# Kernel tuning notes

Hardware: AMD Instinct MI355X
Metric: run time of the kernel (lower is better)

Reference implementation:

```python
import jax, jax.numpy as jnp
import numpy as np

DIM = 256
HEADS = 8
WINDOWS = (1, 2, 4)
B, H, W = 1, 64, 64


def _integral(a):
    # double cumsum over last two dims, then zero-pad one row/col at top/left
    s = jnp.cumsum(jnp.cumsum(a, axis=-2), axis=-1)
    pad = [(0, 0)] * (a.ndim - 2) + [(1, 0), (1, 0)]
    return jnp.pad(s, pad)


def _box(P, ws, Ho, Wo):
    # replicate-pad then box-difference; equivalent to the 2x2 [[1,-1],[-1,1]]
    # kernel conv2d with dilation=ws applied in the torch module.
    tp = ws - 1
    r = tp // 2
    l = tp - r
    pad = [(0, 0)] * (P.ndim - 2) + [(l, r), (l, r)]
    Pp = jnp.pad(P, pad, mode='edge')
    return (Pp[..., ws:ws + Ho, ws:ws + Wo] - Pp[..., ws:ws + Ho, :Wo]
            - Pp[..., :Ho, ws:ws + Wo] + Pp[..., :Ho, :Wo])


def setup_inputs() -> dict:
    key = jax.random.key(0)
    ks = jax.random.split(key, 6)
    x = jax.random.normal(ks[0], (B, DIM, H, W), jnp.float32)
    Wq = jax.random.normal(ks[1], (DIM, DIM), jnp.float32) * 0.05
    Wk = jax.random.normal(ks[2], (DIM, DIM), jnp.float32) * 0.05
    Wv = jax.random.normal(ks[3], (DIM, DIM), jnp.float32) * 0.05
    Wout = jax.random.normal(ks[4], (DIM, DIM * len(WINDOWS)), jnp.float32) * 0.05
    bout = jnp.zeros((DIM,), jnp.float32)
    return {"x": x, "Wq": Wq, "Wk": Wk, "Wv": Wv, "Wout": Wout, "bout": bout}


def reference(x, Wq, Wk, Wv, Wout, bout):
    b, C, Hh, Ww = x.shape
    h = HEADS
    d = C // h
    # 1x1 convs (no bias)
    q = jnp.einsum('bchw,oc->bohw', x, Wq).reshape(b * h, d, Hh, Ww)
    k = jnp.einsum('bchw,oc->bohw', x, Wk).reshape(b * h, d, Hh, Ww)
    v = jnp.einsum('bchw,oc->bohw', x, Wv).reshape(b * h, d, Hh, Ww)
    q = jax.nn.sigmoid(q)
    k = jax.nn.sigmoid(k)
    v = v / jnp.maximum(jnp.linalg.norm(v, axis=1, keepdims=True), 1e-12)

    Ik = _integral(k)                                  # (bh, d, H+1, W+1)
    Ikv = _integral(jnp.einsum('bfhw,bghw->bfghw', k, v))  # (bh, d, d, H+1, W+1)

    outs = []
    for w in WINDOWS:
        ws = Hh // w
        wk = _box(Ik, ws, Hh, Ww)    # (bh, d, H, W)
        wkv = _box(Ikv, ws, Hh, Ww)  # (bh, d, d, H, W)
        attn = jnp.einsum('bdhw,bdfhw->bfhw', q, wkv)
        norm = jnp.einsum('bdhw,bdhw->bhw', q, wk)
        attn = attn / (norm[:, None] + 1e-6)
        outs.append(attn.reshape(b, C, Hh, Ww))
    o = jnp.concatenate(outs, axis=1)  # (b, C*len(WINDOWS), H, W)
    return jnp.einsum('bchw,oc->bohw', o, Wout) + bout[None, :, None, None]
```

## Files before the change

### kernel.cpp

```cpp
#include <hip/hip_runtime.h>
#include <math.h>

#define NPIX 4096
#define CHSZ 3145728
#define NRMSZ 98304

template <int CTRL, int RM>
__device__ __forceinline__ float dpp_add(float x) {
    int xi = __builtin_bit_cast(int, x);
    int sh = __builtin_amdgcn_update_dpp(0, xi, CTRL, RM, 0xf, false);
    return x + __builtin_bit_cast(float, sh);
}

__device__ __forceinline__ float wave_iscan(float x) {
    x = dpp_add<0x111, 0xf>(x);
    x = dpp_add<0x112, 0xf>(x);
    x = dpp_add<0x114, 0xf>(x);
    x = dpp_add<0x118, 0xf>(x);
    x = dpp_add<0x142, 0xa>(x);
    x = dpp_add<0x143, 0xc>(x);
    return x;
}

__device__ __forceinline__ void lds_barrier() {
    asm volatile("s_waitcnt lgkmcnt(0)" ::: "memory");
    __builtin_amdgcn_s_barrier();
    __builtin_amdgcn_sched_barrier(0);
}

__global__ __launch_bounds__(256) void qkv_kernel(
    const float* __restrict__ x, const float* __restrict__ Wq,
    const float* __restrict__ Wk, const float* __restrict__ Wv,
    float* __restrict__ qo, float* __restrict__ ko, float* __restrict__ vo)
{
    const int pt = blockIdx.x * 128;
    const int ot = blockIdx.y * 32;
    const int mat = blockIdx.z;
    const float* __restrict__ W = (mat == 0) ? Wq : ((mat == 1) ? Wk : Wv);
    float* __restrict__ out = (mat == 0) ? qo : ((mat == 1) ? ko : vo);

    __shared__ __align__(16) float Xs[32][132];
    __shared__ __align__(16) float Wt[32][36];

    const int t = threadIdx.x;
    const int pc = t & 31;
    const int oc = t >> 5;
    const int xc = t >> 5;
    const int xp = (t & 31) << 2;
    const int lo = t >> 3;
    const int lg = (t & 7) << 2;

    float4 xf[4];
    float4 wf;
#pragma unroll
    for (int i = 0; i < 4; i++)
        xf[i] = *reinterpret_cast<const float4*>(x + (xc + 8 * i) * NPIX + pt + xp);
    wf = *reinterpret_cast<const float4*>(W + (ot + lo) * 256 + lg);

    float acc[4][4];
#pragma unroll
    for (int j = 0; j < 4; j++)
#pragma unroll
        for (int i = 0; i < 4; i++) acc[j][i] = 0.f;

    for (int kt = 0; kt < 256; kt += 32) {
#pragma unroll
        for (int i = 0; i < 4; i++)
            *reinterpret_cast<float4*>(&Xs[xc + 8 * i][xp]) = xf[i];
        Wt[lg + 0][lo] = wf.x;
        Wt[lg + 1][lo] = wf.y;
        Wt[lg + 2][lo] = wf.z;
        Wt[lg + 3][lo] = wf.w;
        __syncthreads();
        if (kt + 32 < 256) {
#pragma unroll
            for (int i = 0; i < 4; i++)
                xf[i] = *reinterpret_cast<const float4*>(
                    x + (kt + 32 + xc + 8 * i) * NPIX + pt + xp);
            wf = *reinterpret_cast<const float4*>(W + (ot + lo) * 256 + kt + 32 + lg);
        }
#pragma unroll
        for (int kk = 0; kk < 32; kk++) {
            float4 a = *reinterpret_cast<const float4*>(&Xs[kk][pc << 2]);
            float av[4] = {a.x, a.y, a.z, a.w};
            float4 b4 = *reinterpret_cast<const float4*>(&Wt[kk][oc << 2]);
            float bv[4] = {b4.x, b4.y, b4.z, b4.w};
#pragma unroll
            for (int j = 0; j < 4; j++)
#pragma unroll
                for (int i = 0; i < 4; i++)
                    acc[j][i] = fmaf(bv[j], av[i], acc[j][i]);
        }
        __syncthreads();
    }

    if (mat < 2) {
#pragma unroll
        for (int j = 0; j < 4; j++) {
            const int o = ot + (oc << 2) + j;
            float4 r;
            r.x = 1.f / (1.f + __expf(-acc[j][0]));
            r.y = 1.f / (1.f + __expf(-acc[j][1]));
            r.z = 1.f / (1.f + __expf(-acc[j][2]));
            r.w = 1.f / (1.f + __expf(-acc[j][3]));
            *reinterpret_cast<float4*>(out + o * NPIX + pt + (pc << 2)) = r;
        }
    } else {
        float* scratch = &Xs[0][0];
        __syncthreads();
#pragma unroll
        for (int i = 0; i < 4; i++) {
            float ss = 0.f;
#pragma unroll
            for (int j = 0; j < 4; j++) ss += acc[j][i] * acc[j][i];
            scratch[oc * 128 + (pc << 2) + i] = ss;
        }
        __syncthreads();
        float scale[4];
#pragma unroll
        for (int i = 0; i < 4; i++) {
            float tot = 0.f;
#pragma unroll
            for (int g = 0; g < 8; g++) tot += scratch[g * 128 + (pc << 2) + i];
            scale[i] = 1.f / fmaxf(sqrtf(tot), 1e-12f);
        }
#pragma unroll
        for (int j = 0; j < 4; j++) {
            const int o = ot + (oc << 2) + j;
            float4 r;
            r.x = acc[j][0] * scale[0];
            r.y = acc[j][1] * scale[1];
            r.z = acc[j][2] * scale[2];
            r.w = acc[j][3] * scale[3];
            *reinterpret_cast<float4*>(out + o * NPIX + pt + (pc << 2)) = r;
        }
    }
}

template <int PD>
__global__ __launch_bounds__(512) void attn_kernel(
    const float* __restrict__ q, const float* __restrict__ k,
    const float* __restrict__ v, float* __restrict__ num, float* __restrict__ nrm)
{
    const int f = blockIdx.x;
    const int head = blockIdx.y;
    const int dg = blockIdx.z;
    const bool isnorm = (f == 32);

    const float* __restrict__ kh = k + (head * 32 + dg * PD) * NPIX;
    const float* __restrict__ qh = q + (head * 32 + dg * PD) * NPIX;
    const float* __restrict__ vf = v + (head * 32 + (isnorm ? 0 : f)) * NPIX;

    __shared__ __align__(16) float Pt[65][132];
    __shared__ float csum[8][68];

    const int t = threadIdx.x;
    const int lane = t & 63;
    const int wv = t >> 6;

    for (int i = t; i < 65 * 132; i += 512) (&Pt[0][0])[i] = 0.f;

    float vreg[8], kcur[8];
#pragma unroll
    for (int i = 0; i < 8; i++) {
        const int r = wv * 8 + i;
        vreg[i] = isnorm ? 1.f : vf[r * 64 + lane];
        kcur[i] = kh[r * 64 + lane];
    }

    float acc[3][8];
#pragma unroll
    for (int w = 0; w < 3; w++)
#pragma unroll
        for (int i = 0; i < 8; i++) acc[w][i] = 0.f;

    lds_barrier();

    for (int dd = 0; dd < PD; dd++) {
        float qv[8];
#pragma unroll
        for (int g = 0; g < 2; g++)
#pragma unroll
            for (int j = 0; j < 4; j++)
                qv[g * 4 + j] = qh[dd * NPIX + ((wv + 8 * g) * 4 + j) * 64 + lane];

        float pv[8];
        float run = 0.f;
#pragma unroll
        for (int i = 0; i < 8; i++) {
            float rs = wave_iscan(kcur[i] * vreg[i]);
            pv[i] = run;
            run += rs;
        }
        if (dd + 1 < PD) {
#pragma unroll
            for (int i = 0; i < 8; i++)
                kcur[i] = kh[(dd + 1) * NPIX + (wv * 8 + i) * 64 + lane];
        }
        csum[wv][lane] = run;
        lds_barrier();
        float off = 0.f;
#pragma unroll
        for (int w2 = 0; w2 < 7; w2++) if (w2 < wv) off += csum[w2][lane];
#pragma unroll
        for (int i = 0; i < 8; i++) pv[i] += off;
#pragma unroll
        for (int s = 0; s < 2; s++) {
            float4 r4 = make_float4(pv[4 * s], pv[4 * s + 1], pv[4 * s + 2], pv[4 * s + 3]);
            *reinterpret_cast<float4*>(&Pt[lane + 1][32 + wv * 8 + 4 * s]) = r4;
        }
        if (wv == 7) {
            const float tot = off + run;
            const float4 p4 = make_float4(tot, tot, tot, tot);
#pragma unroll
            for (int s = 0; s < 8; s++)
                *reinterpret_cast<float4*>(&Pt[lane + 1][96 + 4 * s]) = p4;
        }
        lds_barrier();
#pragma unroll
        for (int g = 0; g < 2; g++) {
            const int y0 = (wv + 8 * g) * 4;
#pragma unroll
            for (int w = 0; w < 3; w++) {
                const int hw = 32 >> w;
                const int xlo = max(lane - hw, 0);
                const int xhi = min(lane + hw, 64);
                const int ylo = 32 + y0 - hw;
                const int yhi = 32 + y0 + hw;
                float4 A4 = *reinterpret_cast<const float4*>(&Pt[xhi][yhi]);
                float4 B4 = *reinterpret_cast<const float4*>(&Pt[xlo][yhi]);
                float4 C4, E4;
                if (y0 + 3 <= hw) {
                    C4 = make_float4(0.f, 0.f, 0.f, 0.f);
                    E4 = C4;
                } else {
                    C4 = *reinterpret_cast<const float4*>(&Pt[xhi][ylo]);
                    E4 = *reinterpret_cast<const float4*>(&Pt[xlo][ylo]);
                }
                acc[w][g * 4 + 0] = fmaf(qv[g * 4 + 0], (A4.x - B4.x) - (C4.x - E4.x), acc[w][g * 4 + 0]);
                acc[w][g * 4 + 1] = fmaf(qv[g * 4 + 1], (A4.y - B4.y) - (C4.y - E4.y), acc[w][g * 4 + 1]);
                acc[w][g * 4 + 2] = fmaf(qv[g * 4 + 2], (A4.z - B4.z) - (C4.z - E4.z), acc[w][g * 4 + 2]);
                acc[w][g * 4 + 3] = fmaf(qv[g * 4 + 3], (A4.w - B4.w) - (C4.w - E4.w), acc[w][g * 4 + 3]);
            }
        }
    }

    float* __restrict__ nout = num + (size_t)dg * CHSZ;
    float* __restrict__ rout = nrm + (size_t)dg * NRMSZ;
#pragma unroll
    for (int w = 0; w < 3; w++) {
#pragma unroll
        for (int g = 0; g < 2; g++) {
#pragma unroll
            for (int j = 0; j < 4; j++) {
                const int px = ((wv + 8 * g) * 4 + j) * 64 + lane;
                const float val = acc[w][g * 4 + j];
                if (isnorm) rout[(w * 8 + head) * NPIX + px] = val;
                else        nout[((w * 8 + head) * 32 + f) * NPIX + px] = val;
            }
        }
    }
}

template <int NS>
__global__ __launch_bounds__(256) void out_kernel(
    const float* __restrict__ num, const float* __restrict__ nrm,
    const float* __restrict__ Wout, float* __restrict__ obuf)
{
    const int pt = blockIdx.x * 64;
    const int ot = blockIdx.y * 64;
    const int kt0 = blockIdx.z * 12;
    __shared__ __align__(16) float As[32][68];
    __shared__ __align__(16) float Wt[32][68];
    const int t = threadIdx.x;
    const int pc = t & 15;
    const int oc = t >> 4;
    const int xc = t >> 4;
    const int xp = (t & 15) << 2;
    const int lo = t & 63;
    const int lc = (t >> 6) << 2;

    float4 nv[NS][2], mv[NS], wf[2];
#pragma unroll
    for (int s = 0; s < NS; s++) {
#pragma unroll
        for (int i = 0; i < 2; i++)
            nv[s][i] = *reinterpret_cast<const float4*>(
                num + (size_t)s * CHSZ + (size_t)(kt0 * 32 + xc + 16 * i) * NPIX + pt + xp);
        mv[s] = *reinterpret_cast<const float4*>(
            nrm + (size_t)s * NRMSZ + kt0 * NPIX + pt + xp);
    }
    wf[0] = *reinterpret_cast<const float4*>(Wout + (ot + lo) * 768 + kt0 * 32 + lc);
    wf[1] = *reinterpret_cast<const float4*>(Wout + (ot + lo) * 768 + kt0 * 32 + lc + 16);

    float acc[4][4];
#pragma unroll
    for (int j = 0; j < 4; j++)
#pragma unroll
        for (int i = 0; i < 4; i++) acc[j][i] = 0.f;

    for (int kt = kt0; kt < kt0 + 12; kt++) {
        float4 ms = mv[0];
#pragma unroll
        for (int s = 1; s < NS; s++) {
            ms.x += mv[s].x; ms.y += mv[s].y; ms.z += mv[s].z; ms.w += mv[s].w;
        }
        float4 rv;
        rv.x = 1.f / (ms.x + 1e-6f); rv.y = 1.f / (ms.y + 1e-6f);
        rv.z = 1.f / (ms.z + 1e-6f); rv.w = 1.f / (ms.w + 1e-6f);
#pragma unroll
        for (int i = 0; i < 2; i++) {
            float4 r = nv[0][i];
#pragma unroll
            for (int s = 1; s < NS; s++) {
                r.x += nv[s][i].x; r.y += nv[s][i].y;
                r.z += nv[s][i].z; r.w += nv[s][i].w;
            }
            r.x *= rv.x; r.y *= rv.y; r.z *= rv.z; r.w *= rv.w;
            *reinterpret_cast<float4*>(&As[xc + 16 * i][xp]) = r;
        }
#pragma unroll
        for (int i = 0; i < 2; i++) {
            Wt[lc + 16 * i + 0][lo] = wf[i].x;
            Wt[lc + 16 * i + 1][lo] = wf[i].y;
            Wt[lc + 16 * i + 2][lo] = wf[i].z;
            Wt[lc + 16 * i + 3][lo] = wf[i].w;
        }
        __syncthreads();
        if (kt + 1 < kt0 + 12) {
#pragma unroll
            for (int s = 0; s < NS; s++) {
#pragma unroll
                for (int i = 0; i < 2; i++)
                    nv[s][i] = *reinterpret_cast<const float4*>(
                        num + (size_t)s * CHSZ +
                        (size_t)((kt + 1) * 32 + xc + 16 * i) * NPIX + pt + xp);
                mv[s] = *reinterpret_cast<const float4*>(
                    nrm + (size_t)s * NRMSZ + (kt + 1) * NPIX + pt + xp);
            }
            wf[0] = *reinterpret_cast<const float4*>(
                Wout + (ot + lo) * 768 + (kt + 1) * 32 + lc);
            wf[1] = *reinterpret_cast<const float4*>(
                Wout + (ot + lo) * 768 + (kt + 1) * 32 + lc + 16);
        }
#pragma unroll
        for (int kk = 0; kk < 32; kk++) {
            float4 a = *reinterpret_cast<const float4*>(&As[kk][pc << 2]);
            float av[4] = {a.x, a.y, a.z, a.w};
            float4 b4 = *reinterpret_cast<const float4*>(&Wt[kk][oc << 2]);
            float bv[4] = {b4.x, b4.y, b4.z, b4.w};
#pragma unroll
            for (int j = 0; j < 4; j++)
#pragma unroll
                for (int i = 0; i < 4; i++)
                    acc[j][i] = fmaf(bv[j], av[i], acc[j][i]);
        }
        __syncthreads();
    }

    float* __restrict__ ob = obuf + (size_t)blockIdx.z * 1048576;
#pragma unroll
    for (int j = 0; j < 4; j++) {
        const int o = ot + (oc << 2) + j;
        float4 r;
        r.x = acc[j][0]; r.y = acc[j][1]; r.z = acc[j][2]; r.w = acc[j][3];
        *reinterpret_cast<float4*>(ob + o * NPIX + pt + (pc << 2)) = r;
    }
}

__global__ __launch_bounds__(256) void kmerge_kernel(
    const float* __restrict__ obuf, const float* __restrict__ bout,
    float* __restrict__ out)
{
    const int i4 = (blockIdx.x * 256 + threadIdx.x) * 4;
    const float bb = bout[i4 >> 12];
    float4 a = *reinterpret_cast<const float4*>(obuf + i4);
    float4 b = *reinterpret_cast<const float4*>(obuf + 1048576 + i4);
    float4 r;
    r.x = a.x + b.x + bb;
    r.y = a.y + b.y + bb;
    r.z = a.z + b.z + bb;
    r.w = a.w + b.w + bb;
    *reinterpret_cast<float4*>(out + i4) = r;
}

extern "C" void kernel_launch(void* const* d_in, const int* in_sizes, int n_in,
                              void* d_out, int out_size, void* d_ws, size_t ws_size,
                              hipStream_t stream)
{
    const float* x    = (const float*)d_in[0];
    const float* Wq   = (const float*)d_in[1];
    const float* Wk   = (const float*)d_in[2];
    const float* Wv   = (const float*)d_in[3];
    const float* Wout = (const float*)d_in[4];
    const float* bout = (const float*)d_in[5];
    float* out = (float*)d_out;

    float* ws = (float*)d_ws;
    float* q   = ws;
    float* k   = ws + 1048576;
    float* v   = ws + 2097152;
    float* num = ws + 3145728;
    float* obuf = ws;
    const size_t fl = ws_size / 4;

    qkv_kernel<<<dim3(32, 8, 3), 256, 0, stream>>>(x, Wq, Wk, Wv, q, k, v);

    if (fl >= 3145728 + (size_t)4 * (CHSZ + NRMSZ)) {
        float* nrm = num + (size_t)4 * CHSZ;
        attn_kernel<8><<<dim3(33, 8, 4), 512, 0, stream>>>(q, k, v, num, nrm);
        out_kernel<4><<<dim3(64, 4, 2), 256, 0, stream>>>(num, nrm, Wout, obuf);
    } else if (fl >= 3145728 + (size_t)2 * (CHSZ + NRMSZ)) {
        float* nrm = num + (size_t)2 * CHSZ;
        attn_kernel<16><<<dim3(33, 8, 2), 512, 0, stream>>>(q, k, v, num, nrm);
        out_kernel<2><<<dim3(64, 4, 2), 256, 0, stream>>>(num, nrm, Wout, obuf);
    } else {
        float* nrm = num + CHSZ;
        attn_kernel<32><<<dim3(33, 8, 1), 512, 0, stream>>>(q, k, v, num, nrm);
        out_kernel<1><<<dim3(64, 4, 2), 256, 0, stream>>>(num, nrm, Wout, obuf);
    }
    kmerge_kernel<<<dim3(1024), 256, 0, stream>>>(obuf, bout, out);
}
```

Measured before the change: 141.7 us.

## Double-buffer prefix tile and software-pipeline scan to drop one barrier per step

The LDS prefix-sum tile and the column-sum scratch are double-buffered. The scan for step dd+1 is computed while step dd's box sums are read, which removes one workgroup barrier per iteration. The padded 132-wide tile, which replicated the total into 32 columns, is shrunk to 68 columns with a single total column, and the edge cases are handled by explicit branches. The trade is more registers (pvn, runn) and divergent branch paths in the inner loop.

```diff
diff --git a/kernel.cpp b/kernel.cpp
--- a/kernel.cpp
+++ b/kernel.cpp
@@ -151,14 +151,14 @@
     const float* __restrict__ qh = q + (head * 32 + dg * PD) * NPIX;
     const float* __restrict__ vf = v + (head * 32 + (isnorm ? 0 : f)) * NPIX;
 
-    __shared__ __align__(16) float Pt[65][132];
-    __shared__ float csum[8][68];
+    __shared__ __align__(16) float Pt[2][65][68];
+    __shared__ float csum[2][8][68];
 
     const int t = threadIdx.x;
     const int lane = t & 63;
     const int wv = t >> 6;
 
-    for (int i = t; i < 65 * 132; i += 512) (&Pt[0][0])[i] = 0.f;
+    for (int i = t; i < 2 * 65 * 68; i += 512) (&Pt[0][0][0])[i] = 0.f;
 
     float vreg[8], kcur[8];
 #pragma unroll
@@ -174,17 +174,8 @@
 #pragma unroll
         for (int i = 0; i < 8; i++) acc[w][i] = 0.f;
 
-    lds_barrier();
-
-    for (int dd = 0; dd < PD; dd++) {
-        float qv[8];
-#pragma unroll
-        for (int g = 0; g < 2; g++)
-#pragma unroll
-            for (int j = 0; j < 4; j++)
-                qv[g * 4 + j] = qh[dd * NPIX + ((wv + 8 * g) * 4 + j) * 64 + lane];
-
-        float pv[8];
+    float pv[8], runcur;
+    {
         float run = 0.f;
 #pragma unroll
         for (int i = 0; i < 8; i++) {
@@ -192,29 +183,50 @@
             pv[i] = run;
             run += rs;
         }
+        csum[0][wv][lane] = run;
+        runcur = run;
+        if (PD > 1) {
+#pragma unroll
+            for (int i = 0; i < 8; i++)
+                kcur[i] = kh[1 * NPIX + (wv * 8 + i) * 64 + lane];
+        }
+    }
+    lds_barrier();
+
+    float pvn[8], runn;
+    for (int dd = 0; dd < PD; dd++) {
+        const int b = dd & 1;
+        float off = 0.f;
+#pragma unroll
+        for (int w2 = 0; w2 < 7; w2++) if (w2 < wv) off += csum[b][w2][lane];
+#pragma unroll
+        for (int s = 0; s < 2; s++) {
+            float4 r4 = make_float4(pv[4 * s] + off, pv[4 * s + 1] + off,
+                                    pv[4 * s + 2] + off, pv[4 * s + 3] + off);
+            *reinterpret_cast<float4*>(&Pt[b][lane + 1][wv * 8 + 4 * s]) = r4;
+        }
+        if (wv == 7) Pt[b][lane + 1][64] = off + runcur;
+        float qv[8];
+#pragma unroll
+        for (int g = 0; g < 2; g++)
+#pragma unroll
+            for (int j = 0; j < 4; j++)
+                qv[g * 4 + j] = qh[dd * NPIX + ((wv + 8 * g) * 4 + j) * 64 + lane];
         if (dd + 1 < PD) {
-#pragma unroll
-            for (int i = 0; i < 8; i++)
-                kcur[i] = kh[(dd + 1) * NPIX + (wv * 8 + i) * 64 + lane];
-        }
-        csum[wv][lane] = run;
-        lds_barrier();
-        float off = 0.f;
-#pragma unroll
-        for (int w2 = 0; w2 < 7; w2++) if (w2 < wv) off += csum[w2][lane];
-#pragma unroll
-        for (int i = 0; i < 8; i++) pv[i] += off;
-#pragma unroll
-        for (int s = 0; s < 2; s++) {
-            float4 r4 = make_float4(pv[4 * s], pv[4 * s + 1], pv[4 * s + 2], pv[4 * s + 3]);
-            *reinterpret_cast<float4*>(&Pt[lane + 1][32 + wv * 8 + 4 * s]) = r4;
-        }
-        if (wv == 7) {
-            const float tot = off + run;
-            const float4 p4 = make_float4(tot, tot, tot, tot);
-#pragma unroll
-            for (int s = 0; s < 8; s++)
-                *reinterpret_cast<float4*>(&Pt[lane + 1][96 + 4 * s]) = p4;
+            float run = 0.f;
+#pragma unroll
+            for (int i = 0; i < 8; i++) {
+                float rs = wave_iscan(kcur[i] * vreg[i]);
+                pvn[i] = run;
+                run += rs;
+            }
+            csum[b ^ 1][wv][lane] = run;
+            runn = run;
+            if (dd + 2 < PD) {
+#pragma unroll
+                for (int i = 0; i < 8; i++)
+                    kcur[i] = kh[(dd + 2) * NPIX + (wv * 8 + i) * 64 + lane];
+            }
         }
         lds_barrier();
 #pragma unroll
@@ -225,23 +237,40 @@
                 const int hw = 32 >> w;
                 const int xlo = max(lane - hw, 0);
                 const int xhi = min(lane + hw, 64);
-                const int ylo = 32 + y0 - hw;
-                const int yhi = 32 + y0 + hw;
-                float4 A4 = *reinterpret_cast<const float4*>(&Pt[xhi][yhi]);
-                float4 B4 = *reinterpret_cast<const float4*>(&Pt[xlo][yhi]);
-                float4 C4, E4;
+                float c0, c1, c2, c3;
                 if (y0 + 3 <= hw) {
-                    C4 = make_float4(0.f, 0.f, 0.f, 0.f);
-                    E4 = C4;
+                    float4 A4 = *reinterpret_cast<const float4*>(&Pt[b][xhi][y0 + hw]);
+                    float4 B4 = *reinterpret_cast<const float4*>(&Pt[b][xlo][y0 + hw]);
+                    c0 = A4.x - B4.x; c1 = A4.y - B4.y;
+                    c2 = A4.z - B4.z; c3 = A4.w - B4.w;
+                } else if (y0 + hw >= 64) {
+                    float As = Pt[b][xhi][64];
+                    float Bs = Pt[b][xlo][64];
+                    float4 C4 = *reinterpret_cast<const float4*>(&Pt[b][xhi][y0 - hw]);
+                    float4 E4 = *reinterpret_cast<const float4*>(&Pt[b][xlo][y0 - hw]);
+                    const float ab = As - Bs;
+                    c0 = ab - (C4.x - E4.x); c1 = ab - (C4.y - E4.y);
+                    c2 = ab - (C4.z - E4.z); c3 = ab - (C4.w - E4.w);
                 } else {
-                    C4 = *reinterpret_cast<const float4*>(&Pt[xhi][ylo]);
-                    E4 = *reinterpret_cast<const float4*>(&Pt[xlo][ylo]);
+                    float4 A4 = *reinterpret_cast<const float4*>(&Pt[b][xhi][y0 + hw]);
+                    float4 B4 = *reinterpret_cast<const float4*>(&Pt[b][xlo][y0 + hw]);
+                    float4 C4 = *reinterpret_cast<const float4*>(&Pt[b][xhi][y0 - hw]);
+                    float4 E4 = *reinterpret_cast<const float4*>(&Pt[b][xlo][y0 - hw]);
+                    c0 = (A4.x - B4.x) - (C4.x - E4.x);
+                    c1 = (A4.y - B4.y) - (C4.y - E4.y);
+                    c2 = (A4.z - B4.z) - (C4.z - E4.z);
+                    c3 = (A4.w - B4.w) - (C4.w - E4.w);
                 }
-                acc[w][g * 4 + 0] = fmaf(qv[g * 4 + 0], (A4.x - B4.x) - (C4.x - E4.x), acc[w][g * 4 + 0]);
-                acc[w][g * 4 + 1] = fmaf(qv[g * 4 + 1], (A4.y - B4.y) - (C4.y - E4.y), acc[w][g * 4 + 1]);
-                acc[w][g * 4 + 2] = fmaf(qv[g * 4 + 2], (A4.z - B4.z) - (C4.z - E4.z), acc[w][g * 4 + 2]);
-                acc[w][g * 4 + 3] = fmaf(qv[g * 4 + 3], (A4.w - B4.w) - (C4.w - E4.w), acc[w][g * 4 + 3]);
-            }
+                acc[w][g * 4 + 0] = fmaf(qv[g * 4 + 0], c0, acc[w][g * 4 + 0]);
+                acc[w][g * 4 + 1] = fmaf(qv[g * 4 + 1], c1, acc[w][g * 4 + 1]);
+                acc[w][g * 4 + 2] = fmaf(qv[g * 4 + 2], c2, acc[w][g * 4 + 2]);
+                acc[w][g * 4 + 3] = fmaf(qv[g * 4 + 3], c3, acc[w][g * 4 + 3]);
+            }
+        }
+        if (dd + 1 < PD) {
+#pragma unroll
+            for (int i = 0; i < 8; i++) pv[i] = pvn[i];
+            runcur = runn;
         }
     }
 
```

Measured after the change: 142.5 us. Within noise of the previous version (+0.5%).

## Enlarge output-projection tile and use three-way split-K with a 3-way merge

Applied to the files above, without the earlier changes.

The output projection kernel now computes a 128-pixel by 64-output tile per block, with each thread holding 8x4 accumulators instead of 4x4. The K dimension is split three ways instead of two, and the merge kernel sums three partial buffers. Partial slices of num and nrm are summed as they are loaded, so only the reduced float4 values stay in registers rather than every slice. This aims for more FMA work per LDS load and lower register use for the prefetch buffers, at the cost of more accumulators, fewer blocks (384 vs 512) and an extra partial buffer to read in the merge.

```diff
diff --git a/kernel.cpp b/kernel.cpp
--- a/kernel.cpp
+++ b/kernel.cpp
@@ -267,57 +267,57 @@
     const float* __restrict__ num, const float* __restrict__ nrm,
     const float* __restrict__ Wout, float* __restrict__ obuf)
 {
-    const int pt = blockIdx.x * 64;
+    const int pt = blockIdx.x * 128;
     const int ot = blockIdx.y * 64;
-    const int kt0 = blockIdx.z * 12;
-    __shared__ __align__(16) float As[32][68];
+    const int kt0 = blockIdx.z * 8;
+    __shared__ __align__(16) float As[32][132];
     __shared__ __align__(16) float Wt[32][68];
     const int t = threadIdx.x;
-    const int pc = t & 15;
-    const int oc = t >> 4;
-    const int xc = t >> 4;
-    const int xp = (t & 15) << 2;
+    const int pc = t & 31;
+    const int oc = t >> 5;
+    const int xc = t >> 5;
+    const int xp = (t & 31) << 2;
     const int lo = t & 63;
     const int lc = (t >> 6) << 2;
 
-    float4 nv[NS][2], mv[NS], wf[2];
-#pragma unroll
-    for (int s = 0; s < NS; s++) {
-#pragma unroll
-        for (int i = 0; i < 2; i++)
-            nv[s][i] = *reinterpret_cast<const float4*>(
-                num + (size_t)s * CHSZ + (size_t)(kt0 * 32 + xc + 16 * i) * NPIX + pt + xp);
-        mv[s] = *reinterpret_cast<const float4*>(
+    float4 snv[4], smv, wf[2];
+#pragma unroll
+    for (int i = 0; i < 4; i++) {
+        snv[i] = *reinterpret_cast<const float4*>(
+            num + (size_t)(kt0 * 32 + xc + 8 * i) * NPIX + pt + xp);
+#pragma unroll
+        for (int s = 1; s < NS; s++) {
+            float4 v2 = *reinterpret_cast<const float4*>(
+                num + (size_t)s * CHSZ + (size_t)(kt0 * 32 + xc + 8 * i) * NPIX + pt + xp);
+            snv[i].x += v2.x; snv[i].y += v2.y; snv[i].z += v2.z; snv[i].w += v2.w;
+        }
+    }
+    smv = *reinterpret_cast<const float4*>(nrm + kt0 * NPIX + pt + xp);
+#pragma unroll
+    for (int s = 1; s < NS; s++) {
+        float4 v2 = *reinterpret_cast<const float4*>(
             nrm + (size_t)s * NRMSZ + kt0 * NPIX + pt + xp);
+        smv.x += v2.x; smv.y += v2.y; smv.z += v2.z; smv.w += v2.w;
     }
     wf[0] = *reinterpret_cast<const float4*>(Wout + (ot + lo) * 768 + kt0 * 32 + lc);
     wf[1] = *reinterpret_cast<const float4*>(Wout + (ot + lo) * 768 + kt0 * 32 + lc + 16);
 
-    float acc[4][4];
-#pragma unroll
-    for (int j = 0; j < 4; j++)
+    float acc[8][4];
+#pragma unroll
+    for (int j = 0; j < 8; j++)
 #pragma unroll
         for (int i = 0; i < 4; i++) acc[j][i] = 0.f;
 
-    for (int kt = kt0; kt < kt0 + 12; kt++) {
-        float4 ms = mv[0];
-#pragma unroll
-        for (int s = 1; s < NS; s++) {
-            ms.x += mv[s].x; ms.y += mv[s].y; ms.z += mv[s].z; ms.w += mv[s].w;
-        }
+    for (int kt = kt0; kt < kt0 + 8; kt++) {
         float4 rv;
-        rv.x = 1.f / (ms.x + 1e-6f); rv.y = 1.f / (ms.y + 1e-6f);
-        rv.z = 1.f / (ms.z + 1e-6f); rv.w = 1.f / (ms.w + 1e-6f);
-#pragma unroll
-        for (int i = 0; i < 2; i++) {
-            float4 r = nv[0][i];
-#pragma unroll
-            for (int s = 1; s < NS; s++) {
-                r.x += nv[s][i].x; r.y += nv[s][i].y;
-                r.z += nv[s][i].z; r.w += nv[s][i].w;
-            }
-            r.x *= rv.x; r.y *= rv.y; r.z *= rv.z; r.w *= rv.w;
-            *reinterpret_cast<float4*>(&As[xc + 16 * i][xp]) = r;
+        rv.x = 1.f / (smv.x + 1e-6f); rv.y = 1.f / (smv.y + 1e-6f);
+        rv.z = 1.f / (smv.z + 1e-6f); rv.w = 1.f / (smv.w + 1e-6f);
+#pragma unroll
+        for (int i = 0; i < 4; i++) {
+            float4 r;
+            r.x = snv[i].x * rv.x; r.y = snv[i].y * rv.y;
+            r.z = snv[i].z * rv.z; r.w = snv[i].w * rv.w;
+            *reinterpret_cast<float4*>(&As[xc + 8 * i][xp]) = r;
         }
 #pragma unroll
         for (int i = 0; i < 2; i++) {
@@ -327,16 +327,27 @@
             Wt[lc + 16 * i + 3][lo] = wf[i].w;
         }
         __syncthreads();
-        if (kt + 1 < kt0 + 12) {
-#pragma unroll
-            for (int s = 0; s < NS; s++) {
-#pragma unroll
-                for (int i = 0; i < 2; i++)
-                    nv[s][i] = *reinterpret_cast<const float4*>(
+        if (kt + 1 < kt0 + 8) {
+#pragma unroll
+            for (int i = 0; i < 4; i++) {
+                snv[i] = *reinterpret_cast<const float4*>(
+                    num + (size_t)((kt + 1) * 32 + xc + 8 * i) * NPIX + pt + xp);
+#pragma unroll
+                for (int s = 1; s < NS; s++) {
+                    float4 v2 = *reinterpret_cast<const float4*>(
                         num + (size_t)s * CHSZ +
-                        (size_t)((kt + 1) * 32 + xc + 16 * i) * NPIX + pt + xp);
-                mv[s] = *reinterpret_cast<const float4*>(
+                        (size_t)((kt + 1) * 32 + xc + 8 * i) * NPIX + pt + xp);
+                    snv[i].x += v2.x; snv[i].y += v2.y;
+                    snv[i].z += v2.z; snv[i].w += v2.w;
+                }
+            }
+            smv = *reinterpret_cast<const float4*>(
+                nrm + (kt + 1) * NPIX + pt + xp);
+#pragma unroll
+            for (int s = 1; s < NS; s++) {
+                float4 v2 = *reinterpret_cast<const float4*>(
                     nrm + (size_t)s * NRMSZ + (kt + 1) * NPIX + pt + xp);
+                smv.x += v2.x; smv.y += v2.y; smv.z += v2.z; smv.w += v2.w;
             }
             wf[0] = *reinterpret_cast<const float4*>(
                 Wout + (ot + lo) * 768 + (kt + 1) * 32 + lc);
@@ -347,10 +358,11 @@
         for (int kk = 0; kk < 32; kk++) {
             float4 a = *reinterpret_cast<const float4*>(&As[kk][pc << 2]);
             float av[4] = {a.x, a.y, a.z, a.w};
-            float4 b4 = *reinterpret_cast<const float4*>(&Wt[kk][oc << 2]);
-            float bv[4] = {b4.x, b4.y, b4.z, b4.w};
-#pragma unroll
-            for (int j = 0; j < 4; j++)
+            float4 b0 = *reinterpret_cast<const float4*>(&Wt[kk][oc << 3]);
+            float4 b1 = *reinterpret_cast<const float4*>(&Wt[kk][(oc << 3) + 4]);
+            float bv[8] = {b0.x, b0.y, b0.z, b0.w, b1.x, b1.y, b1.z, b1.w};
+#pragma unroll
+            for (int j = 0; j < 8; j++)
 #pragma unroll
                 for (int i = 0; i < 4; i++)
                     acc[j][i] = fmaf(bv[j], av[i], acc[j][i]);
@@ -360,8 +372,8 @@
 
     float* __restrict__ ob = obuf + (size_t)blockIdx.z * 1048576;
 #pragma unroll
-    for (int j = 0; j < 4; j++) {
-        const int o = ot + (oc << 2) + j;
+    for (int j = 0; j < 8; j++) {
+        const int o = ot + (oc << 3) + j;
         float4 r;
         r.x = acc[j][0]; r.y = acc[j][1]; r.z = acc[j][2]; r.w = acc[j][3];
         *reinterpret_cast<float4*>(ob + o * NPIX + pt + (pc << 2)) = r;
@@ -376,11 +388,12 @@
     const float bb = bout[i4 >> 12];
     float4 a = *reinterpret_cast<const float4*>(obuf + i4);
     float4 b = *reinterpret_cast<const float4*>(obuf + 1048576 + i4);
+    float4 c = *reinterpret_cast<const float4*>(obuf + 2097152 + i4);
     float4 r;
-    r.x = a.x + b.x + bb;
-    r.y = a.y + b.y + bb;
-    r.z = a.z + b.z + bb;
-    r.w = a.w + b.w + bb;
+    r.x = a.x + b.x + c.x + bb;
+    r.y = a.y + b.y + c.y + bb;
+    r.z = a.z + b.z + c.z + bb;
+    r.w = a.w + b.w + c.w + bb;
     *reinterpret_cast<float4*>(out + i4) = r;
 }
 
@@ -409,15 +422,15 @@
     if (fl >= 3145728 + (size_t)4 * (CHSZ + NRMSZ)) {
         float* nrm = num + (size_t)4 * CHSZ;
         attn_kernel<8><<<dim3(33, 8, 4), 512, 0, stream>>>(q, k, v, num, nrm);
-        out_kernel<4><<<dim3(64, 4, 2), 256, 0, stream>>>(num, nrm, Wout, obuf);
+        out_kernel<4><<<dim3(32, 4, 3), 256, 0, stream>>>(num, nrm, Wout, obuf);
     } else if (fl >= 3145728 + (size_t)2 * (CHSZ + NRMSZ)) {
         float* nrm = num + (size_t)2 * CHSZ;
         attn_kernel<16><<<dim3(33, 8, 2), 512, 0, stream>>>(q, k, v, num, nrm);
-        out_kernel<2><<<dim3(64, 4, 2), 256, 0, stream>>>(num, nrm, Wout, obuf);
+        out_kernel<2><<<dim3(32, 4, 3), 256, 0, stream>>>(num, nrm, Wout, obuf);
     } else {
         float* nrm = num + CHSZ;
         attn_kernel<32><<<dim3(33, 8, 1), 512, 0, stream>>>(q, k, v, num, nrm);
-        out_kernel<1><<<dim3(64, 4, 2), 256, 0, stream>>>(num, nrm, Wout, obuf);
+        out_kernel<1><<<dim3(32, 4, 3), 256, 0, stream>>>(num, nrm, Wout, obuf);
     }
     kmerge_kernel<<<dim3(1024), 256, 0, stream>>>(obuf, bout, out);
 }
```

After: 148.0 us. 4.4% more time.
